# Optimization experiments

Hardware: AMD Instinct MI355X
Metric: run time of the kernel (lower is better)

## Reference

```python
import jax, jax.numpy as jnp
import numpy as np

NEG_SLOPE = 0.2  # PyG GATConv default negative_slope


def _gat_dense(x, W, att_src, att_dst, bias):
    """PyG GATConv on a fully-connected graph (self-loops included) == dense attention.
    x: [N, F_in], W: [F_in, H*C], att_src/att_dst: [H, C], bias: [H*C] or [C].
    Returns per-head outputs [N, H, C] (bias added by caller after concat/mean).
    """
    H, C = att_src.shape
    N = x.shape[0]
    h = (x @ W).reshape(N, H, C)                      # transformed node feats
    s = jnp.einsum('nhc,hc->nh', h, att_src)          # alpha_src per source node
    t = jnp.einsum('nhc,hc->nh', h, att_dst)          # alpha_dst per dest node
    # e[i, j, h] = leaky_relu(alpha_dst[i] + alpha_src[j]); softmax over sources j
    e = jax.nn.leaky_relu(t[:, None, :] + s[None, :, :], NEG_SLOPE)  # [N, N, H]
    a = jax.nn.softmax(e, axis=1)
    out = jnp.einsum('ijh,jhc->ihc', a, h)            # aggregate sources -> dest
    return out


def setup_inputs() -> dict:
    key = jax.random.key(0)
    ks = jax.random.split(key, 11)
    N, D, C, H = 4096, 768, 128, 4
    sd1 = 1.0 / np.sqrt(D)
    sd2 = 1.0 / np.sqrt(H * C)
    sd3 = 1.0 / np.sqrt(C)
    return {
        'node_feats': jax.random.normal(ks[0], (N, D), dtype=jnp.float32),
        'W1': jax.random.normal(ks[1], (D, H * C), dtype=jnp.float32) * sd1,
        'att_src1': jax.random.normal(ks[2], (H, C), dtype=jnp.float32) * sd3,
        'att_dst1': jax.random.normal(ks[3], (H, C), dtype=jnp.float32) * sd3,
        'b1': jnp.zeros((H * C,), dtype=jnp.float32),
        'W2': jax.random.normal(ks[4], (H * C, C), dtype=jnp.float32) * sd2,
        'att_src2': jax.random.normal(ks[5], (1, C), dtype=jnp.float32) * sd3,
        'att_dst2': jax.random.normal(ks[6], (1, C), dtype=jnp.float32) * sd3,
        'b2': jnp.zeros((C,), dtype=jnp.float32),
        'fcW': jax.random.normal(ks[7], (C, D), dtype=jnp.float32) * sd3,
        'fcb': jnp.zeros((D,), dtype=jnp.float32),
    }


def reference(node_feats, W1, att_src1, att_dst1, b1, W2, att_src2, att_dst2, b2, fcW, fcb):
    N = node_feats.shape[0]
    # GAT layer 1: 4 heads, concat=True
    x = _gat_dense(node_feats, W1, att_src1, att_dst1, b1).reshape(N, -1) + b1
    x = jax.nn.elu(x)
    # GAT layer 2: 1 head, concat=False (mean over the single head == identity)
    x = _gat_dense(x, W2, att_src2, att_dst2, b2)[:, 0, :] + b2
    x = jax.nn.elu(x)
    x = x.mean(axis=0)            # [gat_hidden]
    return x @ fcW + fcb          # [hidden_dim]
```

## Files before the change

kernel.cpp:

```cpp
#include <hip/hip_runtime.h>
#include <hip/hip_bf16.h>


#define NNODE 4096
#define CDIM 128
#define TW 132
#define NEG 0.2f
#define CHUNK 64
#define NCHUNK 64
#define SEG 8
#define SEGK (NNODE / SEG)

typedef __bf16 bf16x8 __attribute__((ext_vector_type(8)));
typedef float f32x4 __attribute__((ext_vector_type(4)));

__device__ __forceinline__ unsigned short f2b(float f) {
  unsigned int u = __float_as_uint(f);
  u += 0x7fffu + ((u >> 16) & 1u);
  return (unsigned short)(u >> 16);
}

__global__ __launch_bounds__(256) void prep_kernel(const float* __restrict__ x,
                                                   const float* __restrict__ W1,
                                                   const float* __restrict__ W2,
                                                   unsigned short* __restrict__ xb,
                                                   unsigned short* __restrict__ W1t,
                                                   unsigned short* __restrict__ W2t,
                                                   float* __restrict__ zbase) {
  __shared__ float tile[64][65];
  int b = blockIdx.x, t = threadIdx.x;
  if (b < 3072) {
    int i = b * 256 + t;
    float4 v = ((const float4*)x)[i];
    ushort4 o;
    o.x = f2b(v.x); o.y = f2b(v.y); o.z = f2b(v.z); o.w = f2b(v.w);
    ((ushort4*)xb)[i] = o;
    return;
  }
  if (b >= 3072 + 96 + 16) {
    int idx = (b - 3072 - 96 - 16) * 256 + t;
    if (idx < 10272) {
      float4 z = {0.f, 0.f, 0.f, 0.f};
      ((float4*)zbase)[idx] = z;
    }
    return;
  }
  const float* W; unsigned short* Wt; int K, N, n0, k0;
  if (b < 3072 + 96) {
    int b2 = b - 3072; W = W1; Wt = W1t; K = 768; N = 512;
    n0 = (b2 & 7) * 64; k0 = (b2 >> 3) * 64;
  } else {
    int b3 = b - 3072 - 96; W = W2; Wt = W2t; K = 512; N = 128;
    n0 = (b3 & 1) * 64; k0 = (b3 >> 1) * 64;
  }
  for (int p = 0; p < 16; p++) {
    int e = p * 256 + t;
    int rr = e >> 6, cc = e & 63;
    tile[rr][cc] = W[(size_t)(k0 + rr) * N + n0 + cc];
  }
  __syncthreads();
  for (int p = 0; p < 16; p++) {
    int e = p * 256 + t;
    int rr = e >> 6, cc = e & 63;
    Wt[(size_t)(n0 + rr) * K + k0 + cc] = f2b(tile[cc][rr]);
  }
}

template <int BM, int BN>
__global__ __launch_bounds__(256) void mfma_gemm_bt(const unsigned short* __restrict__ A,
                                                    const unsigned short* __restrict__ Bt,
                                                    float* __restrict__ C,
                                                    const float* __restrict__ asrc,
                                                    const float* __restrict__ adst,
                                                    float* __restrict__ s,
                                                    float* __restrict__ t,
                                                    int M, int N, int K) {
  __shared__ __align__(16) unsigned short As[BM * 40];
  __shared__ __align__(16) unsigned short Bs[BN * 40];
  constexpr int WM = BM / 2, WN = BN / 2;
  constexpr int FI = WM / 16, FJ = WN / 16;
  constexpr int EA = BM * 32 / 8;
  constexpr int EB = BN * 32 / 8;
  constexpr int NA = (EA + 255) / 256;
  constexpr int NB = (EB + 255) / 256;
  int tid = threadIdx.x;
  int lane = tid & 63, wave = tid >> 6;
  int wm = (wave >> 1) * WM, wn = (wave & 1) * WN;
  int m0 = blockIdx.y * BM, n0 = blockIdx.x * BN;
  int fm = lane & 15, fq = lane >> 4;
  f32x4 acc[FI][FJ] = {};
  uint4 ar[NA], br[NB];
#pragma unroll
  for (int q = 0; q < NA; q++) {
    int e = q * 256 + tid;
    if (e < EA) {
      int r = e >> 2, kk = (e & 3) * 8;
      ar[q] = *(const uint4*)(A + (size_t)(m0 + r) * K + kk);
    }
  }
#pragma unroll
  for (int q = 0; q < NB; q++) {
    int e = q * 256 + tid;
    if (e < EB) {
      int r = e >> 2, kk = (e & 3) * 8;
      br[q] = *(const uint4*)(Bt + (size_t)(n0 + r) * K + kk);
    }
  }
  for (int k0 = 0; k0 < K; k0 += 32) {
    __syncthreads();
#pragma unroll
    for (int q = 0; q < NA; q++) {
      int e = q * 256 + tid;
      if (e < EA) {
        int r = e >> 2, kk = (e & 3) * 8;
        *(uint4*)&As[r * 40 + kk] = ar[q];
      }
    }
#pragma unroll
    for (int q = 0; q < NB; q++) {
      int e = q * 256 + tid;
      if (e < EB) {
        int r = e >> 2, kk = (e & 3) * 8;
        *(uint4*)&Bs[r * 40 + kk] = br[q];
      }
    }
    __syncthreads();
    if (k0 + 32 < K) {
#pragma unroll
      for (int q = 0; q < NA; q++) {
        int e = q * 256 + tid;
        if (e < EA) {
          int r = e >> 2, kk = (e & 3) * 8;
          ar[q] = *(const uint4*)(A + (size_t)(m0 + r) * K + k0 + 32 + kk);
        }
      }
#pragma unroll
      for (int q = 0; q < NB; q++) {
        int e = q * 256 + tid;
        if (e < EB) {
          int r = e >> 2, kk = (e & 3) * 8;
          br[q] = *(const uint4*)(Bt + (size_t)(n0 + r) * K + k0 + 32 + kk);
        }
      }
    }
    bf16x8 af[FI], bfr[FJ];
#pragma unroll
    for (int i = 0; i < FI; i++)
      af[i] = *(const bf16x8*)&As[(wm + i * 16 + fm) * 40 + fq * 8];
#pragma unroll
    for (int j = 0; j < FJ; j++)
      bfr[j] = *(const bf16x8*)&Bs[(wn + j * 16 + fm) * 40 + fq * 8];
#pragma unroll
    for (int i = 0; i < FI; i++)
#pragma unroll
      for (int j = 0; j < FJ; j++)
        acc[i][j] = __builtin_amdgcn_mfma_f32_16x16x32_bf16(af[i], bfr[j], acc[i][j], 0, 0, 0);
  }
#pragma unroll
  for (int i = 0; i < FI; i++) {
#pragma unroll
    for (int j = 0; j < FJ; j++) {
      int r = m0 + wm + i * 16 + fq * 4;
      int ccol = n0 + wn + j * 16 + fm;
#pragma unroll
      for (int reg = 0; reg < 4; reg++)
        C[(size_t)(r + reg) * N + ccol] = acc[i][j][reg];
    }
  }
  int hh = (n0 + wn) / CDIM;
  float av[FJ], dv[FJ];
#pragma unroll
  for (int j = 0; j < FJ; j++) {
    int col = (n0 + wn + j * 16 + fm) & (CDIM - 1);
    av[j] = asrc[hh * CDIM + col];
    dv[j] = adst[hh * CDIM + col];
  }
#pragma unroll
  for (int i = 0; i < FI; i++) {
#pragma unroll
    for (int reg = 0; reg < 4; reg++) {
      float ssum = 0.f, tsum = 0.f;
#pragma unroll
      for (int j = 0; j < FJ; j++) {
        ssum = fmaf(acc[i][j][reg], av[j], ssum);
        tsum = fmaf(acc[i][j][reg], dv[j], tsum);
      }
#pragma unroll
      for (int o = 1; o < 16; o <<= 1) {
        ssum += __shfl_xor(ssum, o, 64);
        tsum += __shfl_xor(tsum, o, 64);
      }
      if (fm == 0) {
        int r = m0 + wm + i * 16 + fq * 4 + reg;
        atomicAdd(&s[(size_t)hh * NNODE + r], ssum);
        atomicAdd(&t[(size_t)hh * NNODE + r], tsum);
      }
    }
  }
}

__global__ __launch_bounds__(256) void rank_count_kernel(const float* __restrict__ s,
                                                         int* __restrict__ partial) {
  __shared__ __align__(16) float keys[SEGK];
  int hh = blockIdx.z, seg = blockIdx.y, tid = threadIdx.x;
  const float* sp = s + (size_t)hh * NNODE;
  for (int k = tid; k < SEGK; k += 256) keys[k] = sp[seg * SEGK + k];
  __syncthreads();
  int mi = blockIdx.x * 256 + tid;
  float mk = sp[mi];
  int jbase = seg * SEGK;
  int cnt = 0;
#pragma unroll 4
  for (int j = 0; j < SEGK; j += 4) {
    float4 kv = *(const float4*)&keys[j];
    int jj = jbase + j;
    cnt += (kv.x < mk) || (kv.x == mk && (jj + 0) < mi);
    cnt += (kv.y < mk) || (kv.y == mk && (jj + 1) < mi);
    cnt += (kv.z < mk) || (kv.z == mk && (jj + 2) < mi);
    cnt += (kv.w < mk) || (kv.w == mk && (jj + 3) < mi);
  }
  partial[((size_t)hh * SEG + seg) * NNODE + mi] = cnt;
}

__global__ __launch_bounds__(256) void rank_scatter_kernel(const float* __restrict__ s,
                                                           const int* __restrict__ partial,
                                                           float* __restrict__ ss,
                                                           int* __restrict__ si) {
  int hh = blockIdx.y;
  int mi = blockIdx.x * 256 + threadIdx.x;
  int rank = 0;
#pragma unroll
  for (int g = 0; g < SEG; g++) rank += partial[((size_t)hh * SEG + g) * NNODE + mi];
  ss[(size_t)hh * NNODE + rank] = s[(size_t)hh * NNODE + mi];
  si[(size_t)hh * NNODE + rank] = mi;
}

__global__ __launch_bounds__(128) void passA_kernel(const float* __restrict__ h,
                                                    const float* __restrict__ ss,
                                                    const int* __restrict__ si,
                                                    float* __restrict__ partP,
                                                    float* __restrict__ partM, int H) {
  __shared__ float eP[CHUNK], eM[CHUNK];
  __shared__ int ids[CHUNK];
  int b = blockIdx.x, hh = b / NCHUNK, ci = b % NCHUNK;
  int c = threadIdx.x;
  int HC = H * CDIM;
  int base = ci * CHUNK;
  if (c < CHUNK) {
    float sv = ss[(size_t)hh * NNODE + base + c];
    ids[c] = si[(size_t)hh * NNODE + base + c];
    eP[c] = expf(sv);
    eM[c] = expf(NEG * sv);
  }
  __syncthreads();
  float sp = 0.f, sm = 0.f;
  for (int kb = 0; kb < CHUNK; kb += 8) {
    float v[8];
#pragma unroll
    for (int j = 0; j < 8; j++)
      v[j] = h[(size_t)ids[kb + j] * HC + hh * CDIM + c];
#pragma unroll
    for (int j = 0; j < 8; j++) {
      sp = fmaf(eP[kb + j], v[j], sp);
      sm = fmaf(eM[kb + j], v[j], sm);
    }
  }
  size_t o = ((size_t)hh * NCHUNK + ci) * TW;
  partP[o + c] = sp;
  partM[o + c] = sm;
  if (c == 0) {
    float zp = 0.f, zm = 0.f;
#pragma unroll
    for (int k = 0; k < CHUNK; k++) { zp += eP[k]; zm += eM[k]; }
    partP[o + 128] = zp;
    partM[o + 128] = zm;
  }
}

__global__ __launch_bounds__(128) void passC_kernel(const float* __restrict__ h,
                                                    const float* __restrict__ ss,
                                                    const int* __restrict__ si,
                                                    const float* __restrict__ partP,
                                                    const float* __restrict__ partM,
                                                    float* __restrict__ SS,
                                                    float* __restrict__ PP, int H) {
  __shared__ float hrow[CHUNK][CDIM];
  __shared__ float eP[CHUNK], eM[CHUNK];
  __shared__ int ids[CHUNK];
  int b = blockIdx.x, hh = b / NCHUNK, ci = b % NCHUNK;
  int c = threadIdx.x;
  int HC = H * CDIM;
  int base = ci * CHUNK;
  size_t hb = (size_t)hh * (NNODE + 1);
  if (c < CHUNK) {
    float sv = ss[(size_t)hh * NNODE + base + c];
    ids[c] = si[(size_t)hh * NNODE + base + c];
    eP[c] = expf(sv);
    eM[c] = expf(NEG * sv);
  }
  __syncthreads();
  float cm = 0.f, cp = 0.f;
  for (int g0 = 0; g0 < NCHUNK; g0 += 16) {
    float vm[16], vp[16];
#pragma unroll
    for (int j = 0; j < 16; j++) {
      size_t o = ((size_t)hh * NCHUNK + g0 + j) * TW + c;
      vm[j] = partM[o];
      vp[j] = partP[o];
    }
#pragma unroll
    for (int j = 0; j < 16; j++) {
      if (g0 + j < ci) cm += vm[j];
      if (g0 + j > ci) cp += vp[j];
    }
  }
  float zcm = 0.f, zcp = 0.f;
  if (c == 0) {
    for (int g0 = 0; g0 < NCHUNK; g0 += 16) {
      float vm[16], vp[16];
#pragma unroll
      for (int j = 0; j < 16; j++) {
        size_t o = ((size_t)hh * NCHUNK + g0 + j) * TW + 128;
        vm[j] = partM[o];
        vp[j] = partP[o];
      }
#pragma unroll
      for (int j = 0; j < 16; j++) {
        if (g0 + j < ci) zcm += vm[j];
        if (g0 + j > ci) zcp += vp[j];
      }
    }
  }
  for (int kb = 0; kb < CHUNK; kb += 8) {
    float v[8];
#pragma unroll
    for (int j = 0; j < 8; j++)
      v[j] = h[(size_t)ids[kb + j] * HC + hh * CDIM + c];
#pragma unroll
    for (int j = 0; j < 8; j++) hrow[kb + j][c] = v[j];
  }
  float runm = cm, runzm = zcm;
#pragma unroll 8
  for (int k = 0; k < CHUNK; k++) {
    size_t row = (hb + base + k) * TW;
    PP[row + c] = runm;
    if (c == 0) PP[row + 128] = runzm;
    runm = fmaf(eM[k], hrow[k][c], runm);
    runzm += eM[k];
  }
  if (ci == NCHUNK - 1) {
    size_t row = (hb + NNODE) * TW;
    PP[row + c] = runm;
    if (c == 0) PP[row + 128] = runzm;
  }
  float runp = cp, runzp = zcp;
#pragma unroll 8
  for (int k = CHUNK - 1; k >= 0; k--) {
    runp = fmaf(eP[k], hrow[k][c], runp);
    runzp += eP[k];
    size_t row = (hb + base + k) * TW;
    SS[row + c] = runp;
    if (c == 0) SS[row + 128] = runzp;
  }
  if (ci == NCHUNK - 1) {
    size_t row = (hb + NNODE) * TW;
    SS[row + c] = 0.f;
    if (c == 0) SS[row + 128] = 0.f;
  }
}

template <typename OUT, int IPB, bool COLSUM>
__global__ __launch_bounds__(256) void attend_kernel(const float* __restrict__ SS,
                                                     const float* __restrict__ PP,
                                                     const float* __restrict__ ss,
                                                     const float* __restrict__ tt,
                                                     const float* __restrict__ bias,
                                                     OUT* __restrict__ out,
                                                     float* __restrict__ colsum, int H) {
  __shared__ float red[256];
  int half = threadIdx.x >> 7, c = threadIdx.x & 127;
  int base = blockIdx.x * IPB;
  float csum = 0.f;
#pragma unroll
  for (int q = 0; q < IPB / 2; q++) {
    int b = base + q * 2 + half;
    int n = b / H, hh = b % H;
    float tv = tt[(size_t)hh * NNODE + n];
    const float* sp = ss + (size_t)hh * NNODE;
    float thr = -tv;
    int lo = 0, hi = NNODE;
    while (lo < hi) { int mid = (lo + hi) >> 1; if (sp[mid] < thr) lo = mid + 1; else hi = mid; }
    size_t hb = (size_t)hh * (NNODE + 1);
    float wp = expf(tv), wm = expf(NEG * tv);
    float num = wp * SS[(hb + lo) * TW + c] + wm * PP[(hb + lo) * TW + c];
    float Z = wp * SS[(hb + lo) * TW + 128] + wm * PP[(hb + lo) * TW + 128];
    float o = num / Z + bias[hh * CDIM + c];
    float r = (o > 0.f) ? o : (expf(o) - 1.f);
    if constexpr (sizeof(OUT) == 2)
      out[(size_t)n * (H * CDIM) + hh * CDIM + c] = f2b(r);
    else
      out[(size_t)n * (H * CDIM) + hh * CDIM + c] = r;
    if constexpr (COLSUM) csum += r;
  }
  if constexpr (COLSUM) {
    red[threadIdx.x] = csum;
    __syncthreads();
    if (threadIdx.x < 128) atomicAdd(&colsum[c], red[threadIdx.x] + red[threadIdx.x + 128]);
  }
}

__global__ __launch_bounds__(256) void fc_kernel(const float* __restrict__ colsum,
                                                 const float* __restrict__ fcW,
                                                 const float* __restrict__ fcb,
                                                 float* __restrict__ out) {
  int d = blockIdx.x * 256 + threadIdx.x;
  float acc = fcb[d];
  const float invN = 1.f / NNODE;
  for (int c2 = 0; c2 < CDIM; c2++) acc = fmaf(colsum[c2] * invN, fcW[c2 * 768 + d], acc);
  out[d] = acc;
}

extern "C" void kernel_launch(void* const* d_in, const int* in_sizes, int n_in,
                              void* d_out, int out_size, void* d_ws, size_t ws_size,
                              hipStream_t stream) {
  const float* x   = (const float*)d_in[0];
  const float* W1  = (const float*)d_in[1];
  const float* as1 = (const float*)d_in[2];
  const float* ad1 = (const float*)d_in[3];
  const float* b1  = (const float*)d_in[4];
  const float* W2  = (const float*)d_in[5];
  const float* as2 = (const float*)d_in[6];
  const float* ad2 = (const float*)d_in[7];
  const float* b2  = (const float*)d_in[8];
  const float* fcW = (const float*)d_in[9];
  const float* fcb = (const float*)d_in[10];

  float* ws = (float*)d_ws;
  size_t off = 0;
  auto alloc = [&](size_t nfloats) { float* p = ws + off; off += nfloats; return p; };

  float* h1  = alloc((size_t)NNODE * 512);
  float* x2f = alloc((size_t)NNODE * 256 + 64 + 16384);
  float* h2  = alloc((size_t)NNODE * 128);
  float* x3  = alloc((size_t)NNODE * 128);
  float* s1  = alloc((size_t)4 * NNODE);
  float* t1  = alloc((size_t)4 * NNODE);
  float* s2  = alloc(NNODE);
  float* t2  = alloc(NNODE);
  float* mv  = alloc(128);
  float* sS1 = alloc((size_t)4 * NNODE);
  int*   sI1 = (int*)alloc((size_t)4 * NNODE);
  float* SS1 = alloc((size_t)4 * (NNODE + 1) * TW);
  float* PP1 = alloc((size_t)4 * (NNODE + 1) * TW);
  float* pP1 = alloc((size_t)4 * NCHUNK * TW);
  float* pM1 = alloc((size_t)4 * NCHUNK * TW);
  float* sS2 = alloc(NNODE);
  int*   sI2 = (int*)alloc(NNODE);
  float* SS2 = alloc((size_t)(NNODE + 1) * TW);
  float* PP2 = alloc((size_t)(NNODE + 1) * TW);
  float* pP2 = alloc((size_t)NCHUNK * TW);
  float* pM2 = alloc((size_t)NCHUNK * TW);
  int*   rparts = (int*)alloc((size_t)4 * SEG * NNODE);

  unsigned short* xb  = (unsigned short*)PP1;
  unsigned short* W1t = (unsigned short*)SS1;
  unsigned short* x2b = (unsigned short*)x2f;
  unsigned short* W2t = (unsigned short*)(x2f + NNODE * 256 + 64);

  prep_kernel<<<3072 + 96 + 16 + 41, 256, 0, stream>>>(x, W1, W2, xb, W1t, W2t, s1);
  mfma_gemm_bt<64, 64><<<dim3(512 / 64, NNODE / 64), 256, 0, stream>>>(
      xb, W1t, h1, as1, ad1, s1, t1, NNODE, 512, 768);
  rank_count_kernel<<<dim3(NNODE / 256, SEG, 4), 256, 0, stream>>>(s1, rparts);
  rank_scatter_kernel<<<dim3(NNODE / 256, 4), 256, 0, stream>>>(s1, rparts, sS1, sI1);
  passA_kernel<<<4 * NCHUNK, 128, 0, stream>>>(h1, sS1, sI1, pP1, pM1, 4);
  passC_kernel<<<4 * NCHUNK, 128, 0, stream>>>(h1, sS1, sI1, pP1, pM1, SS1, PP1, 4);
  attend_kernel<unsigned short, 4, false><<<NNODE * 4 / 4, 256, 0, stream>>>(
      SS1, PP1, sS1, t1, b1, x2b, nullptr, 4);
  mfma_gemm_bt<32, 64><<<dim3(128 / 64, NNODE / 32), 256, 0, stream>>>(
      x2b, W2t, h2, as2, ad2, s2, t2, NNODE, 128, 512);
  rank_count_kernel<<<dim3(NNODE / 256, SEG, 1), 256, 0, stream>>>(s2, rparts);
  rank_scatter_kernel<<<dim3(NNODE / 256, 1), 256, 0, stream>>>(s2, rparts, sS2, sI2);
  passA_kernel<<<NCHUNK, 128, 0, stream>>>(h2, sS2, sI2, pP2, pM2, 1);
  passC_kernel<<<NCHUNK, 128, 0, stream>>>(h2, sS2, sI2, pP2, pM2, SS2, PP2, 1);
  attend_kernel<float, 8, true><<<NNODE / 8, 256, 0, stream>>>(
      SS2, PP2, sS2, t2, b2, x3, mv, 1);
  fc_kernel<<<3, 256, 0, stream>>>(mv, fcW, fcb, (float*)d_out);
}
```

Baseline: 233.2 us.

## Fuse prefix-sum pass with attention by sorting destination keys alongside sources

The GEMM epilogue now stores negated dst scores, so the rank sort handles the t values in the same launch as the s values (z=8 and z=2). The passC prefix-table kernel and the attend kernel are merged. Each chunk block builds its local prefix sums in shared memory and handles the destinations whose sorted threshold falls in its key range, found by binary search. This removes the large SS/PP global tables and the per-destination global binary search. The cost is load imbalance, since destination counts per chunk vary, and only 64 to 256 blocks are launched.

```diff
diff --git a/kernel.cpp b/kernel.cpp
--- a/kernel.cpp
+++ b/kernel.cpp
@@ -193,17 +193,17 @@
       if (fm == 0) {
         int r = m0 + wm + i * 16 + fq * 4 + reg;
         atomicAdd(&s[(size_t)hh * NNODE + r], ssum);
-        atomicAdd(&t[(size_t)hh * NNODE + r], tsum);
-      }
-    }
-  }
-}
-
-__global__ __launch_bounds__(256) void rank_count_kernel(const float* __restrict__ s,
+        atomicAdd(&t[(size_t)hh * NNODE + r], -tsum);
+      }
+    }
+  }
+}
+
+__global__ __launch_bounds__(256) void rank_count_kernel(const float* __restrict__ keysg,
                                                          int* __restrict__ partial) {
   __shared__ __align__(16) float keys[SEGK];
-  int hh = blockIdx.z, seg = blockIdx.y, tid = threadIdx.x;
-  const float* sp = s + (size_t)hh * NNODE;
+  int z = blockIdx.z, seg = blockIdx.y, tid = threadIdx.x;
+  const float* sp = keysg + (size_t)z * NNODE;
   for (int k = tid; k < SEGK; k += 256) keys[k] = sp[seg * SEGK + k];
   __syncthreads();
   int mi = blockIdx.x * 256 + tid;
@@ -213,26 +213,25 @@
 #pragma unroll 4
   for (int j = 0; j < SEGK; j += 4) {
     float4 kv = *(const float4*)&keys[j];
-    int jj = jbase + j;
-    cnt += (kv.x < mk) || (kv.x == mk && (jj + 0) < mi);
-    cnt += (kv.y < mk) || (kv.y == mk && (jj + 1) < mi);
-    cnt += (kv.z < mk) || (kv.z == mk && (jj + 2) < mi);
-    cnt += (kv.w < mk) || (kv.w == mk && (jj + 3) < mi);
-  }
-  partial[((size_t)hh * SEG + seg) * NNODE + mi] = cnt;
-}
-
-__global__ __launch_bounds__(256) void rank_scatter_kernel(const float* __restrict__ s,
+    cnt += (kv.x < mk) || (kv.x == mk && (jbase + j + 0) < mi);
+    cnt += (kv.y < mk) || (kv.y == mk && (jbase + j + 1) < mi);
+    cnt += (kv.z < mk) || (kv.z == mk && (jbase + j + 2) < mi);
+    cnt += (kv.w < mk) || (kv.w == mk && (jbase + j + 3) < mi);
+  }
+  partial[((size_t)z * SEG + seg) * NNODE + mi] = cnt;
+}
+
+__global__ __launch_bounds__(256) void rank_scatter_kernel(const float* __restrict__ keysg,
                                                            const int* __restrict__ partial,
                                                            float* __restrict__ ss,
                                                            int* __restrict__ si) {
-  int hh = blockIdx.y;
+  int z = blockIdx.y;
   int mi = blockIdx.x * 256 + threadIdx.x;
   int rank = 0;
 #pragma unroll
-  for (int g = 0; g < SEG; g++) rank += partial[((size_t)hh * SEG + g) * NNODE + mi];
-  ss[(size_t)hh * NNODE + rank] = s[(size_t)hh * NNODE + mi];
-  si[(size_t)hh * NNODE + rank] = mi;
+  for (int g = 0; g < SEG; g++) rank += partial[((size_t)z * SEG + g) * NNODE + mi];
+  ss[(size_t)z * NNODE + rank] = keysg[(size_t)z * NNODE + mi];
+  si[(size_t)z * NNODE + rank] = mi;
 }
 
 __global__ __launch_bounds__(128) void passA_kernel(const float* __restrict__ h,
@@ -277,29 +276,35 @@
   }
 }
 
-__global__ __launch_bounds__(128) void passC_kernel(const float* __restrict__ h,
-                                                    const float* __restrict__ ss,
-                                                    const int* __restrict__ si,
-                                                    const float* __restrict__ partP,
-                                                    const float* __restrict__ partM,
-                                                    float* __restrict__ SS,
-                                                    float* __restrict__ PP, int H) {
-  __shared__ float hrow[CHUNK][CDIM];
-  __shared__ float eP[CHUNK], eM[CHUNK];
+template <typename OUT, int H, int SUBS, bool COLSUM>
+__global__ __launch_bounds__(128) void fused_attend_kernel(
+    const float* __restrict__ h,
+    const float* __restrict__ sS, const int* __restrict__ sI,
+    const float* __restrict__ sT, const int* __restrict__ iT,
+    const float* __restrict__ partP, const float* __restrict__ partM,
+    const float* __restrict__ bias, OUT* __restrict__ out,
+    float* __restrict__ colsum) {
+  __shared__ float PMp[CHUNK + 1][CDIM];
+  __shared__ float PPp[CHUNK + 1][CDIM];
+  __shared__ float keys[CHUNK], ePl[CHUNK], eMl[CHUNK];
   __shared__ int ids[CHUNK];
-  int b = blockIdx.x, hh = b / NCHUNK, ci = b % NCHUNK;
+  __shared__ float zMp[CHUNK + 1], zPp[CHUNK + 1];
+  __shared__ float totzp_sh;
+  int bx = blockIdx.x;
+  int ci = bx / SUBS, sub = bx % SUBS;
+  int hh = blockIdx.y;
   int c = threadIdx.x;
   int HC = H * CDIM;
   int base = ci * CHUNK;
-  size_t hb = (size_t)hh * (NNODE + 1);
   if (c < CHUNK) {
-    float sv = ss[(size_t)hh * NNODE + base + c];
-    ids[c] = si[(size_t)hh * NNODE + base + c];
-    eP[c] = expf(sv);
-    eM[c] = expf(NEG * sv);
+    float sv = sS[(size_t)hh * NNODE + base + c];
+    ids[c] = sI[(size_t)hh * NNODE + base + c];
+    keys[c] = sv;
+    ePl[c] = expf(sv);
+    eMl[c] = expf(NEG * sv);
   }
   __syncthreads();
-  float cm = 0.f, cp = 0.f;
+  float cmM = 0.f, cmP = 0.f, totP = 0.f;
   for (int g0 = 0; g0 < NCHUNK; g0 += 16) {
     float vm[16], vp[16];
 #pragma unroll
@@ -310,11 +315,11 @@
     }
 #pragma unroll
     for (int j = 0; j < 16; j++) {
-      if (g0 + j < ci) cm += vm[j];
-      if (g0 + j > ci) cp += vp[j];
-    }
-  }
-  float zcm = 0.f, zcp = 0.f;
+      totP += vp[j];
+      if (g0 + j < ci) { cmM += vm[j]; cmP += vp[j]; }
+    }
+  }
+  float zcM = 0.f, zcP = 0.f, totZP = 0.f;
   if (c == 0) {
     for (int g0 = 0; g0 < NCHUNK; g0 += 16) {
       float vm[16], vp[16];
@@ -326,86 +331,77 @@
       }
 #pragma unroll
       for (int j = 0; j < 16; j++) {
-        if (g0 + j < ci) zcm += vm[j];
-        if (g0 + j > ci) zcp += vp[j];
-      }
-    }
-  }
+        totZP += vp[j];
+        if (g0 + j < ci) { zcM += vm[j]; zcP += vp[j]; }
+      }
+    }
+  }
+  float runm = cmM, runp = cmP;
   for (int kb = 0; kb < CHUNK; kb += 8) {
     float v[8];
 #pragma unroll
     for (int j = 0; j < 8; j++)
       v[j] = h[(size_t)ids[kb + j] * HC + hh * CDIM + c];
 #pragma unroll
-    for (int j = 0; j < 8; j++) hrow[kb + j][c] = v[j];
-  }
-  float runm = cm, runzm = zcm;
-#pragma unroll 8
-  for (int k = 0; k < CHUNK; k++) {
-    size_t row = (hb + base + k) * TW;
-    PP[row + c] = runm;
-    if (c == 0) PP[row + 128] = runzm;
-    runm = fmaf(eM[k], hrow[k][c], runm);
-    runzm += eM[k];
-  }
-  if (ci == NCHUNK - 1) {
-    size_t row = (hb + NNODE) * TW;
-    PP[row + c] = runm;
-    if (c == 0) PP[row + 128] = runzm;
-  }
-  float runp = cp, runzp = zcp;
-#pragma unroll 8
-  for (int k = CHUNK - 1; k >= 0; k--) {
-    runp = fmaf(eP[k], hrow[k][c], runp);
-    runzp += eP[k];
-    size_t row = (hb + base + k) * TW;
-    SS[row + c] = runp;
-    if (c == 0) SS[row + 128] = runzp;
-  }
-  if (ci == NCHUNK - 1) {
-    size_t row = (hb + NNODE) * TW;
-    SS[row + c] = 0.f;
-    if (c == 0) SS[row + 128] = 0.f;
-  }
-}
-
-template <typename OUT, int IPB, bool COLSUM>
-__global__ __launch_bounds__(256) void attend_kernel(const float* __restrict__ SS,
-                                                     const float* __restrict__ PP,
-                                                     const float* __restrict__ ss,
-                                                     const float* __restrict__ tt,
-                                                     const float* __restrict__ bias,
-                                                     OUT* __restrict__ out,
-                                                     float* __restrict__ colsum, int H) {
-  __shared__ float red[256];
-  int half = threadIdx.x >> 7, c = threadIdx.x & 127;
-  int base = blockIdx.x * IPB;
+    for (int j = 0; j < 8; j++) {
+      int k = kb + j;
+      PMp[k][c] = runm;
+      PPp[k][c] = runp;
+      runm = fmaf(eMl[k], v[j], runm);
+      runp = fmaf(ePl[k], v[j], runp);
+    }
+  }
+  PMp[CHUNK][c] = runm;
+  PPp[CHUNK][c] = runp;
+  if (c == 0) {
+    float zrm = zcM, zrp = zcP;
+    for (int k = 0; k < CHUNK; k++) {
+      zMp[k] = zrm; zPp[k] = zrp;
+      zrm += eMl[k]; zrp += ePl[k];
+    }
+    zMp[CHUNK] = zrm; zPp[CHUNK] = zrp;
+    totzp_sh = totZP;
+  }
+  __syncthreads();
+  float totZPl = totzp_sh;
+  const float* sTp = sT + (size_t)hh * NNODE;
+  const int* iTp = iT + (size_t)hh * NNODE;
+  float loKey = (ci > 0) ? sS[(size_t)hh * NNODE + base - 1] : -3.4e38f;
+  int lo = 0, hi = NNODE;
+  while (lo < hi) { int mid = (lo + hi) >> 1; if (sTp[mid] <= loKey) lo = mid + 1; else hi = mid; }
+  int pLo = lo;
+  int pHi;
+  if (ci == NCHUNK - 1) pHi = NNODE;
+  else {
+    float hiKey = keys[CHUNK - 1];
+    lo = pLo; hi = NNODE;
+    while (lo < hi) { int mid = (lo + hi) >> 1; if (sTp[mid] <= hiKey) lo = mid + 1; else hi = mid; }
+    pHi = lo;
+  }
+  int R = pHi - pLo;
+  int per = (R + SUBS - 1) / SUBS;
+  int myLo = pLo + sub * per;
+  int myHi = myLo + per < pHi ? myLo + per : pHi;
+  float bval = bias[hh * CDIM + c];
   float csum = 0.f;
-#pragma unroll
-  for (int q = 0; q < IPB / 2; q++) {
-    int b = base + q * 2 + half;
-    int n = b / H, hh = b % H;
-    float tv = tt[(size_t)hh * NNODE + n];
-    const float* sp = ss + (size_t)hh * NNODE;
-    float thr = -tv;
-    int lo = 0, hi = NNODE;
-    while (lo < hi) { int mid = (lo + hi) >> 1; if (sp[mid] < thr) lo = mid + 1; else hi = mid; }
-    size_t hb = (size_t)hh * (NNODE + 1);
-    float wp = expf(tv), wm = expf(NEG * tv);
-    float num = wp * SS[(hb + lo) * TW + c] + wm * PP[(hb + lo) * TW + c];
-    float Z = wp * SS[(hb + lo) * TW + 128] + wm * PP[(hb + lo) * TW + 128];
-    float o = num / Z + bias[hh * CDIM + c];
+  for (int p = myLo; p < myHi; p++) {
+    float thr = sTp[p];
+    int n = iTp[p];
+    int l = 0, hh2 = CHUNK;
+    while (l < hh2) { int mid = (l + hh2) >> 1; if (keys[mid] < thr) l = mid + 1; else hh2 = mid; }
+    float wp = expf(-thr), wm = expf(-NEG * thr);
+    float num = wp * (totP - PPp[l][c]) + wm * PMp[l][c];
+    float Z = wp * (totZPl - zPp[l]) + wm * zMp[l];
+    float o = num / Z + bval;
     float r = (o > 0.f) ? o : (expf(o) - 1.f);
     if constexpr (sizeof(OUT) == 2)
-      out[(size_t)n * (H * CDIM) + hh * CDIM + c] = f2b(r);
+      out[(size_t)n * HC + hh * CDIM + c] = f2b(r);
     else
-      out[(size_t)n * (H * CDIM) + hh * CDIM + c] = r;
+      out[(size_t)n * HC + hh * CDIM + c] = r;
     if constexpr (COLSUM) csum += r;
   }
   if constexpr (COLSUM) {
-    red[threadIdx.x] = csum;
-    __syncthreads();
-    if (threadIdx.x < 128) atomicAdd(&colsum[c], red[threadIdx.x] + red[threadIdx.x + 128]);
+    if (myHi > myLo) atomicAdd(&colsum[c], csum);
   }
 }
 
@@ -448,41 +444,39 @@
   float* s2  = alloc(NNODE);
   float* t2  = alloc(NNODE);
   float* mv  = alloc(128);
-  float* sS1 = alloc((size_t)4 * NNODE);
-  int*   sI1 = (int*)alloc((size_t)4 * NNODE);
-  float* SS1 = alloc((size_t)4 * (NNODE + 1) * TW);
-  float* PP1 = alloc((size_t)4 * (NNODE + 1) * TW);
+  float* sA1 = alloc((size_t)8 * NNODE);
+  int*   iA1 = (int*)alloc((size_t)8 * NNODE);
   float* pP1 = alloc((size_t)4 * NCHUNK * TW);
   float* pM1 = alloc((size_t)4 * NCHUNK * TW);
-  float* sS2 = alloc(NNODE);
-  int*   sI2 = (int*)alloc(NNODE);
-  float* SS2 = alloc((size_t)(NNODE + 1) * TW);
-  float* PP2 = alloc((size_t)(NNODE + 1) * TW);
+  float* sA2 = alloc((size_t)2 * NNODE);
+  int*   iA2 = (int*)alloc((size_t)2 * NNODE);
   float* pP2 = alloc((size_t)NCHUNK * TW);
   float* pM2 = alloc((size_t)NCHUNK * TW);
-  int*   rparts = (int*)alloc((size_t)4 * SEG * NNODE);
-
-  unsigned short* xb  = (unsigned short*)PP1;
-  unsigned short* W1t = (unsigned short*)SS1;
+  int*   rparts = (int*)alloc((size_t)8 * SEG * NNODE);
+  float* xbf = alloc((size_t)NNODE * 384);
+  float* w1f = alloc((size_t)512 * 384);
+
+  unsigned short* xb  = (unsigned short*)xbf;
+  unsigned short* W1t = (unsigned short*)w1f;
   unsigned short* x2b = (unsigned short*)x2f;
   unsigned short* W2t = (unsigned short*)(x2f + NNODE * 256 + 64);
 
   prep_kernel<<<3072 + 96 + 16 + 41, 256, 0, stream>>>(x, W1, W2, xb, W1t, W2t, s1);
   mfma_gemm_bt<64, 64><<<dim3(512 / 64, NNODE / 64), 256, 0, stream>>>(
       xb, W1t, h1, as1, ad1, s1, t1, NNODE, 512, 768);
-  rank_count_kernel<<<dim3(NNODE / 256, SEG, 4), 256, 0, stream>>>(s1, rparts);
-  rank_scatter_kernel<<<dim3(NNODE / 256, 4), 256, 0, stream>>>(s1, rparts, sS1, sI1);
-  passA_kernel<<<4 * NCHUNK, 128, 0, stream>>>(h1, sS1, sI1, pP1, pM1, 4);
-  passC_kernel<<<4 * NCHUNK, 128, 0, stream>>>(h1, sS1, sI1, pP1, pM1, SS1, PP1, 4);
-  attend_kernel<unsigned short, 4, false><<<NNODE * 4 / 4, 256, 0, stream>>>(
-      SS1, PP1, sS1, t1, b1, x2b, nullptr, 4);
+  rank_count_kernel<<<dim3(NNODE / 256, SEG, 8), 256, 0, stream>>>(s1, rparts);
+  rank_scatter_kernel<<<dim3(NNODE / 256, 8), 256, 0, stream>>>(s1, rparts, sA1, iA1);
+  passA_kernel<<<4 * NCHUNK, 128, 0, stream>>>(h1, sA1, iA1, pP1, pM1, 4);
+  fused_attend_kernel<unsigned short, 4, 1, false><<<dim3(NCHUNK, 4), 128, 0, stream>>>(
+      h1, sA1, iA1, sA1 + (size_t)4 * NNODE, iA1 + (size_t)4 * NNODE,
+      pP1, pM1, b1, x2b, nullptr);
   mfma_gemm_bt<32, 64><<<dim3(128 / 64, NNODE / 32), 256, 0, stream>>>(
       x2b, W2t, h2, as2, ad2, s2, t2, NNODE, 128, 512);
-  rank_count_kernel<<<dim3(NNODE / 256, SEG, 1), 256, 0, stream>>>(s2, rparts);
-  rank_scatter_kernel<<<dim3(NNODE / 256, 1), 256, 0, stream>>>(s2, rparts, sS2, sI2);
-  passA_kernel<<<NCHUNK, 128, 0, stream>>>(h2, sS2, sI2, pP2, pM2, 1);
-  passC_kernel<<<NCHUNK, 128, 0, stream>>>(h2, sS2, sI2, pP2, pM2, SS2, PP2, 1);
-  attend_kernel<float, 8, true><<<NNODE / 8, 256, 0, stream>>>(
-      SS2, PP2, sS2, t2, b2, x3, mv, 1);
+  rank_count_kernel<<<dim3(NNODE / 256, SEG, 2), 256, 0, stream>>>(s2, rparts);
+  rank_scatter_kernel<<<dim3(NNODE / 256, 2), 256, 0, stream>>>(s2, rparts, sA2, iA2);
+  passA_kernel<<<NCHUNK, 128, 0, stream>>>(h2, sA2, iA2, pP2, pM2, 1);
+  fused_attend_kernel<float, 1, 4, true><<<dim3(NCHUNK * 4, 1), 128, 0, stream>>>(
+      h2, sA2, iA2, sA2 + (size_t)NNODE, iA2 + (size_t)NNODE,
+      pP2, pM2, b2, x3, mv);
   fc_kernel<<<3, 256, 0, stream>>>(mv, fcW, fcb, (float*)d_out);
 }
```

After: 865.8 us. +271.4%, slower.
